# Kernel tuning notes

Hardware: AMD Instinct MI355X
Metric: run time of the kernel (lower is better)

Reference implementation:

```python
import jax, jax.numpy as jnp
import numpy as np

B, S, D, H = 4, 2048, 768, 12
DK = D // H


def setup_inputs() -> dict:
    key = jax.random.key(0)
    ks = jax.random.split(key, 12)
    s = 1.0 / np.sqrt(D)
    return {
        "query": jax.random.normal(ks[0], (B, S, D), jnp.float32),
        "key_": jax.random.normal(ks[1], (B, S, D), jnp.float32),
        "value": jax.random.normal(ks[2], (B, S, D), jnp.float32),
        "mask": jax.random.randint(ks[3], (B, S), 0, 2, jnp.int32),
        # nn.Linear weights are (out_features, in_features); y = x @ W.T + b
        "Wq": jax.random.normal(ks[4], (D, D), jnp.float32) * s,
        "bq": jnp.zeros((D,), jnp.float32),
        "Wk": jax.random.normal(ks[5], (D, D), jnp.float32) * s,
        "bk": jnp.zeros((D,), jnp.float32),
        "Wv": jax.random.normal(ks[6], (D, D), jnp.float32) * s,
        "bv": jnp.zeros((D,), jnp.float32),
        "Wo": jax.random.normal(ks[7], (D, D), jnp.float32) * s,
        "bo": jnp.zeros((D,), jnp.float32),
    }


def reference(query, key_, value, mask, Wq, bq, Wk, bk, Wv, bv, Wo, bo):
    b = query.shape[0]
    # QKV projections, split heads: (B, S, D) -> (B, H, S, DK)
    def proj(x, W, bia):
        y = x @ W.T + bia
        return y.reshape(b, -1, H, DK).transpose(0, 2, 1, 3)

    q = proj(query, Wq, bq)
    k = proj(key_, Wk, bk)
    v = proj(value, Wv, bv)

    # Scaled dot-product attention with full [B, H, S, S] score matrix
    scores = jnp.einsum("bhqd,bhkd->bhqk", q, k) / jnp.sqrt(jnp.float32(DK))
    # mask: (B, S) broadcast over heads and query positions; masked_fill(mask==0, -1e9)
    scores = jnp.where(mask[:, None, None, :] == 0, jnp.float32(-1e9), scores)
    attn = jax.nn.softmax(scores, axis=-1)
    x = jnp.einsum("bhqk,bhkd->bhqd", attn, v)  # (B, H, S, DK)

    # merge heads and output projection
    x = x.transpose(0, 2, 1, 3).reshape(b, -1, H * DK)
    return x @ Wo.T + bo
```

## Files before the change

### kernel.cpp

```cpp
#include <hip/hip_runtime.h>
#include <math.h>

#define B_  4
#define S_  2048
#define D_  768
#define H_  12
#define DK_ 64
#define M_  (B_ * S_)
#define NBH_ (B_ * H_)

typedef float f32x4 __attribute__((ext_vector_type(4)));
typedef float f32x16 __attribute__((ext_vector_type(16)));
typedef __bf16 bf16x8 __attribute__((ext_vector_type(8)));
typedef unsigned u32x4v __attribute__((ext_vector_type(4)));

#if __has_builtin(__builtin_amdgcn_exp2f)
#define EXP2(x) __builtin_amdgcn_exp2f(x)
#else
#define EXP2(x) exp2f(x)
#endif

static __device__ __forceinline__ unsigned short f2bf(float f) {
    unsigned u = __builtin_bit_cast(unsigned, f);
    u += 0x7fffu + ((u >> 16) & 1u);
    return (unsigned short)(u >> 16);
}

static __device__ __forceinline__ unsigned cvt_pk_bf16(float lo, float hi) {
    unsigned r;
    asm("v_cvt_pk_bf16_f32 %0, %1, %2" : "=v"(r) : "v"(lo), "v"(hi));
    return r;
}

static __device__ __forceinline__ void gload_lds16(const void* g, void* l) {
    __builtin_amdgcn_global_load_lds(
        (const __attribute__((address_space(1))) void*)g,
        (__attribute__((address_space(3))) void*)l, 16, 0, 0);
}

__global__ __launch_bounds__(256) void cvt_all(
    const float* __restrict__ q, const float* __restrict__ k,
    const float* __restrict__ v,
    const float* __restrict__ wq, const float* __restrict__ wk,
    const float* __restrict__ wv, const float* __restrict__ wo,
    unsigned short* __restrict__ q16, unsigned short* __restrict__ k16,
    unsigned short* __restrict__ v16,
    unsigned short* __restrict__ wq16, unsigned short* __restrict__ wk16,
    unsigned short* __restrict__ wv16, unsigned short* __restrict__ wo16)
{
    const int z = blockIdx.y;
    const float* src =
        (z == 0) ? q : (z == 1) ? k : (z == 2) ? v :
        (z == 3) ? wq : (z == 4) ? wk : (z == 5) ? wv : wo;
    unsigned short* dst =
        (z == 0) ? q16 : (z == 1) ? k16 : (z == 2) ? v16 :
        (z == 3) ? wq16 : (z == 4) ? wk16 : (z == 5) ? wv16 : wo16;
    const int NG = ((z < 3) ? M_ : D_) * 96;
    for (int g = blockIdx.x * 256 + threadIdx.x; g < NG; g += gridDim.x * 256) {
        int r = g / 96, c8 = g - r * 96;
        int kt = c8 >> 2, sl = c8 & 3;
        const float* sp = src + (size_t)r * D_ + kt * 32 + sl * 8;
        float4 a = *(const float4*)sp;
        float4 b = *(const float4*)(sp + 4);
        u32x4v o;
        o.x = cvt_pk_bf16(a.x, a.y); o.y = cvt_pk_bf16(a.z, a.w);
        o.z = cvt_pk_bf16(b.x, b.y); o.w = cvt_pk_bf16(b.z, b.w);
        *(u32x4v*)(dst + (size_t)r * D_ + kt * 32 + ((sl ^ (r & 3)) << 3)) = o;
    }
}

static __device__ __forceinline__ void gemm_body_dma(
    const unsigned short* __restrict__ A16, const unsigned short* __restrict__ B16,
    const float* __restrict__ bias, void* __restrict__ outp, const int mode,
    const float oscale)
{
    __shared__ __align__(16) unsigned short As[2][128 * 32];
    __shared__ __align__(16) unsigned short Bs[2][128 * 32];

    const int t  = threadIdx.x;
    const int l  = t & 63;
    const int w  = t >> 6;
    const int lr = l & 15;
    const int lg = l >> 4;
    const int wm = w >> 1;
    const int wn = w & 1;
    const int m0 = blockIdx.x * 128;
    const int n0 = blockIdx.y * 128;

    const unsigned short* adma = A16 + (size_t)(m0 + 32 * w + (l >> 2)) * D_ + (l & 3) * 8;
    const unsigned short* bdma = B16 + (size_t)(n0 + 32 * w + (l >> 2)) * D_ + (l & 3) * 8;

#define GSTAGE(K0, NB) do { \
        gload_lds16(adma + (K0),           &As[NB][(32 * w) * 32]); \
        gload_lds16(adma + (K0) + 16 * D_, &As[NB][(32 * w + 16) * 32]); \
        gload_lds16(bdma + (K0),           &Bs[NB][(32 * w) * 32]); \
        gload_lds16(bdma + (K0) + 16 * D_, &Bs[NB][(32 * w + 16) * 32]); \
    } while (0)

    f32x4 acc[4][4];
#pragma unroll
    for (int mi = 0; mi < 4; mi++)
#pragma unroll
        for (int ni = 0; ni < 4; ni++) acc[mi][ni] = (f32x4){0.f, 0.f, 0.f, 0.f};

    const int fsw = lr & 3;

    GSTAGE(0, 0);
    __syncthreads();

    for (int kt = 0; kt < 24; kt++) {
        const int cur = kt & 1;
        if (kt < 23) {
            if (cur) GSTAGE((kt + 1) * 32, 0);
            else     GSTAGE((kt + 1) * 32, 1);
        }

        bf16x8 af[4], bfr[4];
#pragma unroll
        for (int mi = 0; mi < 4; mi++) {
            int row = wm * 64 + mi * 16 + lr;
            af[mi] = *(const bf16x8*)&As[cur][row * 32 + ((lg ^ fsw) << 3)];
        }
#pragma unroll
        for (int ni = 0; ni < 4; ni++) {
            int row = wn * 64 + ni * 16 + lr;
            bfr[ni] = *(const bf16x8*)&Bs[cur][row * 32 + ((lg ^ fsw) << 3)];
        }
#pragma unroll
        for (int mi = 0; mi < 4; mi++)
#pragma unroll
            for (int ni = 0; ni < 4; ni++)
                acc[mi][ni] = __builtin_amdgcn_mfma_f32_16x16x32_bf16(
                    af[mi], bfr[ni], acc[mi][ni], 0, 0, 0);

        __syncthreads();
    }
#undef GSTAGE

    const int mrow0 = m0 + wm * 64;
    const int ncol0 = n0 + wn * 64;
    if (mode == 1) {
        float* out = (float*)outp;
#pragma unroll
        for (int mi = 0; mi < 4; mi++)
#pragma unroll
            for (int ni = 0; ni < 4; ni++) {
                int n = ncol0 + ni * 16 + lr;
                float bv = bias[n];
#pragma unroll
                for (int j = 0; j < 4; j++) {
                    int m = mrow0 + mi * 16 + 4 * lg + j;
                    out[(size_t)m * D_ + n] = acc[mi][ni][j] + bv;
                }
            }
    } else if (mode == 2) {
        unsigned short* out = (unsigned short*)outp;
#pragma unroll
        for (int mi = 0; mi < 4; mi++)
#pragma unroll
            for (int ni = 0; ni < 4; ni++) {
                int n = ncol0 + ni * 16 + lr;
                int h = n >> 6, dk = n & 63;
                float bv = bias[n];
                int m = mrow0 + mi * 16 + 4 * lg;
                int b = m >> 11, s = m & (S_ - 1);
                int slotp = ((s >> 3) & 7) ^ (dk & 7);
                int ssw = (s & ~63) | (slotp << 3) | (s & 7);
                uint2 o;
                o.x = cvt_pk_bf16(acc[mi][ni][0] + bv, acc[mi][ni][1] + bv);
                o.y = cvt_pk_bf16(acc[mi][ni][2] + bv, acc[mi][ni][3] + bv);
                *(uint2*)&out[((size_t)(b * H_ + h) * DK_ + dk) * S_ + ssw] = o;
            }
    } else {
        unsigned short* out = (unsigned short*)outp;
#pragma unroll
        for (int mi = 0; mi < 4; mi++)
#pragma unroll
            for (int ni = 0; ni < 4; ni++) {
                int n = ncol0 + ni * 16 + lr;
                int h = n >> 6, dk = n & 63;
                float bv = bias[n];
#pragma unroll
                for (int j = 0; j < 4; j++) {
                    int m = mrow0 + mi * 16 + 4 * lg + j;
                    int b = m >> 11, s = m & (S_ - 1);
                    int dko = (mode == 3)
                        ? ((dk & 7) | ((((dk >> 3) ^ (s & 7))) << 3)) : dk;
                    out[((size_t)(b * H_ + h) * S_ + s) * DK_ + dko] =
                        f2bf((acc[mi][ni][j] + bv) * oscale);
                }
            }
    }
}

__global__ __launch_bounds__(256) void gemm_qkv(
    const unsigned short* __restrict__ q16, const unsigned short* __restrict__ k16,
    const unsigned short* __restrict__ v16,
    const unsigned short* __restrict__ wq16, const unsigned short* __restrict__ wk16,
    const unsigned short* __restrict__ wv16,
    const float* __restrict__ bq, const float* __restrict__ bk,
    const float* __restrict__ bv,
    unsigned short* __restrict__ Qb, unsigned short* __restrict__ Kb,
    unsigned short* __restrict__ VT)
{
    const int z = blockIdx.z;
    const unsigned short* A = (z == 0) ? q16 : (z == 1) ? k16 : v16;
    const unsigned short* W = (z == 0) ? wq16 : (z == 1) ? wk16 : wv16;
    const float* bias = (z == 0) ? bq : (z == 1) ? bk : bv;
    void* out = (z == 0) ? (void*)Qb : (z == 1) ? (void*)Kb : (void*)VT;
    const int mode = (z == 0) ? 0 : (z == 1) ? 3 : 2;
    const float osc = (z == 0) ? 0.18033688011112042f : 1.0f;
    gemm_body_dma(A, W, bias, out, mode, osc);
}

__global__ __launch_bounds__(256) void gemm_o(
    const unsigned short* __restrict__ X16, const unsigned short* __restrict__ wo16,
    const float* __restrict__ bo, float* __restrict__ out)
{
    gemm_body_dma(X16, wo16, bo, (void*)out, 1, 1.0f);
}

__global__ __launch_bounds__(256) void attn_mfma(
    const unsigned short* __restrict__ Qb, const unsigned short* __restrict__ Kb,
    const unsigned short* __restrict__ VTb, const int* __restrict__ mask,
    unsigned short* __restrict__ Xb16)
{
    __shared__ __align__(16) unsigned short Ks[2][64 * 64];
    __shared__ __align__(16) unsigned short Vs[2][64 * 64];

    const int tid = threadIdx.x;
    const int w  = tid >> 6;
    const int l  = tid & 63;
    const int q  = l & 31;
    const int hl = l >> 5;

    const int bh = blockIdx.x % NBH_;
    const int qt = blockIdx.x / NBH_;
    const int b  = bh / H_;
    const int hh = bh - b * H_;
    const int q0 = qt * 128 + w * 32;

    const unsigned short* qp = Qb + ((size_t)bh * S_ + q0 + q) * DK_;
    bf16x8 qf[4];
#pragma unroll
    for (int c = 0; c < 4; c++)
        qf[c] = *(const bf16x8*)(qp + c * 16 + hl * 8);

    const unsigned qext_sel = (hl == 0) ? 0x00003F80u : 0u;
    const unsigned bias_sel = (hl == 0) ? 0x0000C480u : 0u;
    u32x4v qe; qe.x = qext_sel; qe.y = 0u; qe.z = 0u; qe.w = 0u;
    const bf16x8 qf_ext = __builtin_bit_cast(bf16x8, qe);
    u32x4v on; on.x = on.y = on.z = on.w = 0x3F803F80u;
    const bf16x8 vOnes = __builtin_bit_cast(bf16x8, on);

    f32x16 acc0, acc1, accl;
#pragma unroll
    for (int i = 0; i < 16; i++) { acc0[i] = 0.f; acc1[i] = 0.f; accl[i] = 0.f; }

    const unsigned short* kbase = Kb + (size_t)bh * S_ * DK_;
    const unsigned short* vbase = VTb + (size_t)bh * DK_ * S_;
    const int* mbase = mask + b * S_;

    const unsigned short* kdma = kbase + (16 * w) * DK_ + l * 8;
    const unsigned short* vdma0 = vbase + (size_t)(16 * w + (l >> 3)) * S_ + (l & 7) * 8;
    const unsigned short* vdma1 = vdma0 + (size_t)8 * S_;

#define STAGE_DMA(J0, NB) do { \
        gload_lds16(kdma + (size_t)(J0) * DK_,            &Ks[NB][(16 * w) * 64]); \
        gload_lds16(kdma + (size_t)(J0) * DK_ + 8 * DK_,  &Ks[NB][(16 * w + 8) * 64]); \
        gload_lds16(vdma0 + (J0),                         &Vs[NB][(16 * w) * 64]); \
        gload_lds16(vdma1 + (J0),                         &Vs[NB][(16 * w + 8) * 64]); \
    } while (0)

    STAGE_DMA(0, 0);
    __syncthreads();

    const int fsw = (q & 7) << 3;
    const int kr0o = q * 64;
    const int kr1o = (32 + q) * 64;

    for (int tt = 0; tt < 32; tt++) {
        const int j0  = tt * 64;
        const int cur = tt & 1;

        if (tt < 31) {
            if (cur) STAGE_DMA(j0 + 64, 0); else STAGE_DMA(j0 + 64, 1);
        }

        int mv0 = mbase[j0 + q];
        int mv1 = mbase[j0 + 32 + q];
        u32x4v bw0; bw0.x = (mv0 == 0) ? bias_sel : 0u; bw0.y = 0u; bw0.z = 0u; bw0.w = 0u;
        u32x4v bw1; bw1.x = (mv1 == 0) ? bias_sel : 0u; bw1.y = 0u; bw1.z = 0u; bw1.w = 0u;
        bf16x8 kExt0 = __builtin_bit_cast(bf16x8, bw0);
        bf16x8 kExt1 = __builtin_bit_cast(bf16x8, bw1);

        f32x16 s0, s1;
#pragma unroll
        for (int i = 0; i < 16; i++) { s0[i] = 0.f; s1[i] = 0.f; }
        s0 = __builtin_amdgcn_mfma_f32_32x32x16_bf16(kExt0, qf_ext, s0, 0, 0, 0);
        s1 = __builtin_amdgcn_mfma_f32_32x32x16_bf16(kExt1, qf_ext, s1, 0, 0, 0);
#pragma unroll
        for (int c = 0; c < 4; c++) {
            bf16x8 k0 = *(const bf16x8*)&Ks[cur][kr0o + ((c * 16 + hl * 8) ^ fsw)];
            bf16x8 k1 = *(const bf16x8*)&Ks[cur][kr1o + ((c * 16 + hl * 8) ^ fsw)];
            s0 = __builtin_amdgcn_mfma_f32_32x32x16_bf16(k0, qf[c], s0, 0, 0, 0);
            s1 = __builtin_amdgcn_mfma_f32_32x32x16_bf16(k1, qf[c], s1, 0, 0, 0);
        }

#pragma unroll
        for (int r = 0; r < 16; r++) s0[r] = EXP2(s0[r]);
#pragma unroll
        for (int r = 0; r < 16; r++) s1[r] = EXP2(s1[r]);

#define SVAL(CP, I) (((CP) >> 1) ? s1[I] : s0[I])
        bf16x8 pb[4];
#pragma unroll
        for (int cp = 0; cp < 4; cp++) {
            const int e0 = 8 * (cp & 1);
            unsigned lo0 = cvt_pk_bf16(SVAL(cp, e0 + 0), SVAL(cp, e0 + 1));
            unsigned hi0 = cvt_pk_bf16(SVAL(cp, e0 + 2), SVAL(cp, e0 + 3));
            unsigned lo1 = cvt_pk_bf16(SVAL(cp, e0 + 4), SVAL(cp, e0 + 5));
            unsigned hi1 = cvt_pk_bf16(SVAL(cp, e0 + 6), SVAL(cp, e0 + 7));
            asm("v_permlane32_swap_b32 %0, %1" : "+v"(lo0), "+v"(lo1));
            asm("v_permlane32_swap_b32 %0, %1" : "+v"(hi0), "+v"(hi1));
            u32x4v pw;
            pw.x = lo0; pw.y = hi0; pw.z = lo1; pw.w = hi1;
            pb[cp] = __builtin_bit_cast(bf16x8, pw);
        }
#undef SVAL

#pragma unroll
        for (int cp = 0; cp < 4; cp++) {
            bf16x8 v0 = *(const bf16x8*)&Vs[cur][kr0o + ((cp * 16 + hl * 8) ^ fsw)];
            bf16x8 v1 = *(const bf16x8*)&Vs[cur][kr1o + ((cp * 16 + hl * 8) ^ fsw)];
            acc0 = __builtin_amdgcn_mfma_f32_32x32x16_bf16(v0, pb[cp], acc0, 0, 0, 0);
            acc1 = __builtin_amdgcn_mfma_f32_32x32x16_bf16(v1, pb[cp], acc1, 0, 0, 0);
            accl = __builtin_amdgcn_mfma_f32_32x32x16_bf16(vOnes, pb[cp], accl, 0, 0, 0);
        }

        __syncthreads();
    }
#undef STAGE_DMA

    float inv = 1.f / accl[0];
    unsigned short* ob = Xb16 + ((size_t)b * S_ + q0 + q) * D_ + hh * DK_;
    const int rsw = q & 3;
#pragma unroll
    for (int b2 = 0; b2 < 4; b2++) {
        uint2 o0;
        o0.x = cvt_pk_bf16(acc0[4 * b2 + 0] * inv, acc0[4 * b2 + 1] * inv);
        o0.y = cvt_pk_bf16(acc0[4 * b2 + 2] * inv, acc0[4 * b2 + 3] * inv);
        *(uint2*)(ob + (((b2 ^ rsw) << 3) + 4 * hl)) = o0;
        uint2 o1;
        o1.x = cvt_pk_bf16(acc1[4 * b2 + 0] * inv, acc1[4 * b2 + 1] * inv);
        o1.y = cvt_pk_bf16(acc1[4 * b2 + 2] * inv, acc1[4 * b2 + 3] * inv);
        *(uint2*)(ob + 32 + (((b2 ^ rsw) << 3) + 4 * hl)) = o1;
    }
}

extern "C" void kernel_launch(void* const* d_in, const int* in_sizes, int n_in,
                              void* d_out, int out_size, void* d_ws, size_t ws_size,
                              hipStream_t stream) {
    (void)in_sizes; (void)n_in; (void)out_size; (void)ws_size;

    const float* query = (const float*)d_in[0];
    const float* key_  = (const float*)d_in[1];
    const float* value = (const float*)d_in[2];
    const int*   mask  = (const int*)d_in[3];
    const float* Wq = (const float*)d_in[4];  const float* bq = (const float*)d_in[5];
    const float* Wk = (const float*)d_in[6];  const float* bk = (const float*)d_in[7];
    const float* Wv = (const float*)d_in[8];  const float* bv = (const float*)d_in[9];
    const float* Wo = (const float*)d_in[10]; const float* bo = (const float*)d_in[11];
    float* out = (float*)d_out;

    const size_t MD = (size_t)M_ * D_;
    const size_t DD = (size_t)D_ * D_;
    unsigned short* q16  = (unsigned short*)d_ws;
    unsigned short* k16  = q16 + MD;
    unsigned short* v16  = k16 + MD;
    unsigned short* Qb   = v16 + MD;
    unsigned short* Kb   = Qb + MD;
    unsigned short* VT   = Kb + MD;
    unsigned short* Xb16 = VT + MD;
    unsigned short* Wq16 = Xb16 + MD;
    unsigned short* Wk16 = Wq16 + DD;
    unsigned short* Wv16 = Wk16 + DD;
    unsigned short* Wo16 = Wv16 + DD;

    cvt_all<<<dim3(1024, 7), 256, 0, stream>>>(
        query, key_, value, Wq, Wk, Wv, Wo,
        q16, k16, v16, Wq16, Wk16, Wv16, Wo16);

    gemm_qkv<<<dim3(M_ / 128, D_ / 128, 3), 256, 0, stream>>>(
        q16, k16, v16, Wq16, Wk16, Wv16, bq, bk, bv, Qb, Kb, VT);

    attn_mfma<<<dim3((S_ / 128) * NBH_), 256, 0, stream>>>(Qb, Kb, VT, mask, Xb16);

    gemm_o<<<dim3(M_ / 128, D_ / 128), 256, 0, stream>>>(Xb16, Wo16, bo, out);
}
```

Measured before the change: 174.2 us.

## Triple-buffer K/V LDS staging with partial vmcnt waits and preloaded mask bits

The attention kernel moves from double to triple buffering of K and V tiles in LDS. It prefetches two tiles ahead and replaces the full __syncthreads with an s_waitcnt vmcnt(4) plus a raw barrier, so only the older tile's DMA has to land before each iteration. The whole mask row is also loaded once up front and packed into bitmasks, which removes a global load from every iteration. In exchange the kernel uses more LDS, which may lower occupancy, and the result now depends on hand-counted vmcnt values being correct.

```diff
diff --git a/kernel.cpp b/kernel.cpp
--- a/kernel.cpp
+++ b/kernel.cpp
@@ -225,8 +225,8 @@
     const unsigned short* __restrict__ VTb, const int* __restrict__ mask,
     unsigned short* __restrict__ Xb16)
 {
-    __shared__ __align__(16) unsigned short Ks[2][64 * 64];
-    __shared__ __align__(16) unsigned short Vs[2][64 * 64];
+    __shared__ __align__(16) unsigned short Ks[3][64 * 64];
+    __shared__ __align__(16) unsigned short Vs[3][64 * 64];
 
     const int tid = threadIdx.x;
     const int w  = tid >> 6;
@@ -272,25 +272,43 @@
         gload_lds16(vdma1 + (J0),                         &Vs[NB][(16 * w + 8) * 64]); \
     } while (0)
 
+    int mraw0[32], mraw1[32];
+#pragma unroll
+    for (int t = 0; t < 32; t++) {
+        mraw0[t] = mbase[t * 64 + q];
+        mraw1[t] = mbase[t * 64 + 32 + q];
+    }
     STAGE_DMA(0, 0);
-    __syncthreads();
+    STAGE_DMA(64, 1);
+    unsigned mq0 = 0, mq1 = 0;
+#pragma unroll
+    for (int t = 0; t < 32; t++) {
+        mq0 |= (mraw0[t] == 0 ? 1u : 0u) << t;
+        mq1 |= (mraw1[t] == 0 ? 1u : 0u) << t;
+    }
+    asm volatile("s_waitcnt vmcnt(4)" ::: "memory");
+    __builtin_amdgcn_s_barrier();
+    __builtin_amdgcn_sched_barrier(0);
 
     const int fsw = (q & 7) << 3;
     const int kr0o = q * 64;
     const int kr1o = (32 + q) * 64;
 
     for (int tt = 0; tt < 32; tt++) {
-        const int j0  = tt * 64;
-        const int cur = tt & 1;
-
-        if (tt < 31) {
-            if (cur) STAGE_DMA(j0 + 64, 0); else STAGE_DMA(j0 + 64, 1);
-        }
-
-        int mv0 = mbase[j0 + q];
-        int mv1 = mbase[j0 + 32 + q];
-        u32x4v bw0; bw0.x = (mv0 == 0) ? bias_sel : 0u; bw0.y = 0u; bw0.z = 0u; bw0.w = 0u;
-        u32x4v bw1; bw1.x = (mv1 == 0) ? bias_sel : 0u; bw1.y = 0u; bw1.z = 0u; bw1.w = 0u;
+        const int cur = tt % 3;
+
+        if (tt < 30) {
+            const int j2 = (tt + 2) * 64;
+            const int nb = (tt + 2) % 3;
+            if (nb == 0)      STAGE_DMA(j2, 0);
+            else if (nb == 1) STAGE_DMA(j2, 1);
+            else              STAGE_DMA(j2, 2);
+        }
+
+        u32x4v bw0; bw0.x = ((mq0 >> tt) & 1u) ? bias_sel : 0u;
+        bw0.y = 0u; bw0.z = 0u; bw0.w = 0u;
+        u32x4v bw1; bw1.x = ((mq1 >> tt) & 1u) ? bias_sel : 0u;
+        bw1.y = 0u; bw1.z = 0u; bw1.w = 0u;
         bf16x8 kExt0 = __builtin_bit_cast(bf16x8, bw0);
         bf16x8 kExt1 = __builtin_bit_cast(bf16x8, bw1);
 
@@ -338,7 +356,12 @@
             accl = __builtin_amdgcn_mfma_f32_32x32x16_bf16(vOnes, pb[cp], accl, 0, 0, 0);
         }
 
-        __syncthreads();
+        if (tt < 31) {
+            if (tt <= 29) asm volatile("s_waitcnt vmcnt(4)" ::: "memory");
+            else          asm volatile("s_waitcnt vmcnt(0)" ::: "memory");
+            __builtin_amdgcn_s_barrier();
+            __builtin_amdgcn_sched_barrier(0);
+        }
     }
 #undef STAGE_DMA
 
```

New measurement: 178.9 us. +2.7%, slower.

## Split attention over two key halves and combine partials in separate kernel

Applied to the files above, without the earlier changes.

The attention kernel now splits the 2048 keys into two halves, doubling the grid so each block processes 16 key tiles instead of 32. Each block writes an unnormalized bf16 partial output and its row-sum denominator. A new combine kernel adds the two partials and divides by the summed denominators before the output projection. The aim is more parallelism and shorter per-block serial loops. The cost is an extra launch, extra global traffic for the partial buffers, and bf16 rounding of unnormalized partials.

```diff
diff --git a/kernel.cpp b/kernel.cpp
--- a/kernel.cpp
+++ b/kernel.cpp
@@ -223,7 +223,8 @@
 __global__ __launch_bounds__(256) void attn_mfma(
     const unsigned short* __restrict__ Qb, const unsigned short* __restrict__ Kb,
     const unsigned short* __restrict__ VTb, const int* __restrict__ mask,
-    unsigned short* __restrict__ Xb16)
+    unsigned short* __restrict__ Oa, unsigned short* __restrict__ Ob,
+    float* __restrict__ lA, float* __restrict__ lB)
 {
     __shared__ __align__(16) unsigned short Ks[2][64 * 64];
     __shared__ __align__(16) unsigned short Vs[2][64 * 64];
@@ -234,11 +235,14 @@
     const int q  = l & 31;
     const int hl = l >> 5;
 
-    const int bh = blockIdx.x % NBH_;
-    const int qt = blockIdx.x / NBH_;
+    const int bh   = blockIdx.x % NBH_;
+    const int rest = blockIdx.x / NBH_;
+    const int kh   = rest & 1;
+    const int qt   = rest >> 1;
     const int b  = bh / H_;
     const int hh = bh - b * H_;
     const int q0 = qt * 128 + w * 32;
+    const int koff = kh * 1024;
 
     const unsigned short* qp = Qb + ((size_t)bh * S_ + q0 + q) * DK_;
     bf16x8 qf[4];
@@ -272,18 +276,18 @@
         gload_lds16(vdma1 + (J0),                         &Vs[NB][(16 * w + 8) * 64]); \
     } while (0)
 
-    STAGE_DMA(0, 0);
+    STAGE_DMA(koff, 0);
     __syncthreads();
 
     const int fsw = (q & 7) << 3;
     const int kr0o = q * 64;
     const int kr1o = (32 + q) * 64;
 
-    for (int tt = 0; tt < 32; tt++) {
-        const int j0  = tt * 64;
+    for (int tt = 0; tt < 16; tt++) {
+        const int j0  = koff + tt * 64;
         const int cur = tt & 1;
 
-        if (tt < 31) {
+        if (tt < 15) {
             if (cur) STAGE_DMA(j0 + 64, 0); else STAGE_DMA(j0 + 64, 1);
         }
 
@@ -342,19 +346,56 @@
     }
 #undef STAGE_DMA
 
-    float inv = 1.f / accl[0];
-    unsigned short* ob = Xb16 + ((size_t)b * S_ + q0 + q) * D_ + hh * DK_;
+    unsigned short* obuf = kh ? Ob : Oa;
+    unsigned short* ob = obuf + ((size_t)b * S_ + q0 + q) * D_ + hh * DK_;
     const int rsw = q & 3;
 #pragma unroll
     for (int b2 = 0; b2 < 4; b2++) {
         uint2 o0;
-        o0.x = cvt_pk_bf16(acc0[4 * b2 + 0] * inv, acc0[4 * b2 + 1] * inv);
-        o0.y = cvt_pk_bf16(acc0[4 * b2 + 2] * inv, acc0[4 * b2 + 3] * inv);
+        o0.x = cvt_pk_bf16(acc0[4 * b2 + 0], acc0[4 * b2 + 1]);
+        o0.y = cvt_pk_bf16(acc0[4 * b2 + 2], acc0[4 * b2 + 3]);
         *(uint2*)(ob + (((b2 ^ rsw) << 3) + 4 * hl)) = o0;
         uint2 o1;
-        o1.x = cvt_pk_bf16(acc1[4 * b2 + 0] * inv, acc1[4 * b2 + 1] * inv);
-        o1.y = cvt_pk_bf16(acc1[4 * b2 + 2] * inv, acc1[4 * b2 + 3] * inv);
+        o1.x = cvt_pk_bf16(acc1[4 * b2 + 0], acc1[4 * b2 + 1]);
+        o1.y = cvt_pk_bf16(acc1[4 * b2 + 2], acc1[4 * b2 + 3]);
         *(uint2*)(ob + 32 + (((b2 ^ rsw) << 3) + 4 * hl)) = o1;
+    }
+    if (hl == 0) {
+        float* lp = kh ? lB : lA;
+        lp[(size_t)bh * S_ + q0 + q] = accl[0];
+    }
+}
+
+__global__ __launch_bounds__(256) void combine(
+    const unsigned short* __restrict__ Oa, const unsigned short* __restrict__ Ob,
+    const float* __restrict__ lA, const float* __restrict__ lB,
+    unsigned short* __restrict__ X16)
+{
+    const int NG = M_ * 96;
+    for (int g = blockIdx.x * 256 + threadIdx.x; g < NG; g += gridDim.x * 256) {
+        size_t base = (size_t)g * 8;
+        int row = g / 96;
+        int col8 = g - row * 96;
+        int h = col8 >> 3;
+        int b = row >> 11, s = row & (S_ - 1);
+        size_t li = (size_t)(b * H_ + h) * S_ + s;
+        float inv = 1.f / (lA[li] + lB[li]);
+        u32x4v va = *(const u32x4v*)(Oa + base);
+        u32x4v vb = *(const u32x4v*)(Ob + base);
+        u32x4v o;
+#pragma unroll
+        for (int i = 0; i < 4; i++) {
+            unsigned ua = (i == 0) ? va.x : (i == 1) ? va.y : (i == 2) ? va.z : va.w;
+            unsigned ub = (i == 0) ? vb.x : (i == 1) ? vb.y : (i == 2) ? vb.z : vb.w;
+            float a0 = __builtin_bit_cast(float, (ua & 0xFFFFu) << 16);
+            float a1 = __builtin_bit_cast(float, ua & 0xFFFF0000u);
+            float b0 = __builtin_bit_cast(float, (ub & 0xFFFFu) << 16);
+            float b1 = __builtin_bit_cast(float, ub & 0xFFFF0000u);
+            unsigned r = cvt_pk_bf16((a0 + b0) * inv, (a1 + b1) * inv);
+            if (i == 0) o.x = r; else if (i == 1) o.y = r;
+            else if (i == 2) o.z = r; else o.w = r;
+        }
+        *(u32x4v*)(X16 + base) = o;
     }
 }
 
@@ -387,6 +428,11 @@
     unsigned short* Wv16 = Wk16 + DD;
     unsigned short* Wo16 = Wv16 + DD;
 
+    unsigned short* Oa = q16;
+    unsigned short* Ob = k16;
+    float* lA = (float*)v16;
+    float* lB = lA + (size_t)NBH_ * S_;
+
     cvt_all<<<dim3(1024, 7), 256, 0, stream>>>(
         query, key_, value, Wq, Wk, Wv, Wo,
         q16, k16, v16, Wq16, Wk16, Wv16, Wo16);
@@ -394,7 +440,10 @@
     gemm_qkv<<<dim3(M_ / 128, D_ / 128, 3), 256, 0, stream>>>(
         q16, k16, v16, Wq16, Wk16, Wv16, bq, bk, bv, Qb, Kb, VT);
 
-    attn_mfma<<<dim3((S_ / 128) * NBH_), 256, 0, stream>>>(Qb, Kb, VT, mask, Xb16);
+    attn_mfma<<<dim3(2 * (S_ / 128) * NBH_), 256, 0, stream>>>(
+        Qb, Kb, VT, mask, Oa, Ob, lA, lB);
+
+    combine<<<dim3(2048), 256, 0, stream>>>(Oa, Ob, lA, lB, Xb16);
 
     gemm_o<<<dim3(M_ / 128, D_ / 128), 256, 0, stream>>>(Xb16, Wo16, bo, out);
 }
```

New measurement: 180.9 us. +3.9%, slower.
